# Optimization experiments

Hardware: AMD Instinct MI355X
Metric: run time of the kernel (lower is better)

The kernel has to match this reference:

```python
import jax, jax.numpy as jnp
import numpy as np
from jax import lax

EMBED = 768
D_INNER = 2 * EMBED          # expand = 2
D_STATE = 16
D_CONV = 4
DT_RANK = (EMBED + 15) // 16  # 48
FF = 3072
B, L = 2, 1024


def setup_inputs() -> dict:
    key = jax.random.key(0)
    ks = jax.random.split(key, 20)
    s = 0.02
    inp = {
        "x": jax.random.normal(ks[0], (B, L, EMBED), jnp.float32),
        # Mamba params
        "in_proj_w": jax.random.normal(ks[1], (2 * D_INNER, EMBED), jnp.float32) * s,
        "conv_w": jax.random.normal(ks[2], (D_INNER, 1, D_CONV), jnp.float32) * s,
        "conv_b": jnp.zeros((D_INNER,), jnp.float32),
        "x_proj_w": jax.random.normal(ks[3], (DT_RANK + 2 * D_STATE, D_INNER), jnp.float32) * s,
        "dt_proj_w": jax.random.normal(ks[4], (D_INNER, DT_RANK), jnp.float32) * s,
        "dt_proj_b": jax.random.normal(ks[5], (D_INNER,), jnp.float32) * s,
        "A_log": jnp.log(jnp.broadcast_to(jnp.arange(1, D_STATE + 1, dtype=jnp.float32), (D_INNER, D_STATE))),
        "D_param": jnp.ones((D_INNER,), jnp.float32),
        "out_proj_w": jax.random.normal(ks[6], (EMBED, D_INNER), jnp.float32) * s,
        # block params
        "ln1_w": jnp.ones((EMBED,), jnp.float32), "ln1_b": jnp.zeros((EMBED,), jnp.float32),
        "ln2_w": jnp.ones((EMBED,), jnp.float32), "ln2_b": jnp.zeros((EMBED,), jnp.float32),
        "ffn_w1": jax.random.normal(ks[7], (FF, EMBED), jnp.float32) * s,
        "ffn_b1": jnp.zeros((FF,), jnp.float32),
        "ffn_w2": jax.random.normal(ks[8], (EMBED, FF), jnp.float32) * s,
        "ffn_b2": jnp.zeros((EMBED,), jnp.float32),
    }
    return inp


def _layernorm(x, w, b, eps=1e-5):
    mu = jnp.mean(x, -1, keepdims=True)
    var = jnp.mean((x - mu) ** 2, -1, keepdims=True)
    return (x - mu) * lax.rsqrt(var + eps) * w + b


def _mamba(x, in_proj_w, conv_w, conv_b, x_proj_w, dt_proj_w, dt_proj_b,
           A_log, D_param, out_proj_w):
    # x: [B, L, E]
    xz = jnp.einsum('ble,de->bld', x, in_proj_w)          # [B,L,2*Di]
    xin, z = jnp.split(xz, 2, axis=-1)                    # [B,L,Di] each
    # causal depthwise conv over time
    xc = lax.conv_general_dilated(
        xin.transpose(0, 2, 1), conv_w, window_strides=(1,),
        padding=[(D_CONV - 1, 0)], feature_group_count=D_INNER,
        dimension_numbers=('NCH', 'OIH', 'NCH'))
    xc = (xc + conv_b[None, :, None]).transpose(0, 2, 1)  # [B,L,Di]
    xc = jax.nn.silu(xc)
    # input-dependent SSM params
    x_dbl = jnp.einsum('bld,rd->blr', xc, x_proj_w)       # [B,L,dt_rank+2n]
    dt, Bm, Cm = jnp.split(x_dbl, [DT_RANK, DT_RANK + D_STATE], axis=-1)
    delta = jax.nn.softplus(jnp.einsum('blr,dr->bld', dt, dt_proj_w) + dt_proj_b)
    A = -jnp.exp(A_log)                                   # [Di, n]
    deltaA = jnp.exp(jnp.einsum('bld,dn->bldn', delta, A))
    deltaBu = jnp.einsum('bld,bln,bld->bldn', delta, Bm, xc)

    def step(h, xs):
        dA, dBu, Ct = xs                                  # [B,Di,n],[B,Di,n],[B,n]
        h = dA * h + dBu
        y = jnp.einsum('bdn,bn->bd', h, Ct)
        return h, y

    h0 = jnp.zeros((x.shape[0], D_INNER, D_STATE), x.dtype)
    _, ys = lax.scan(step, h0, (deltaA.transpose(1, 0, 2, 3),
                                deltaBu.transpose(1, 0, 2, 3),
                                Cm.transpose(1, 0, 2)))
    y = ys.transpose(1, 0, 2)                             # [B,L,Di]
    y = y + xc * D_param
    y = y * jax.nn.silu(z)
    return jnp.einsum('bld,ed->ble', y, out_proj_w)


def reference(x, in_proj_w, conv_w, conv_b, x_proj_w, dt_proj_w, dt_proj_b,
              A_log, D_param, out_proj_w, ln1_w, ln1_b, ln2_w, ln2_b,
              ffn_w1, ffn_b1, ffn_w2, ffn_b2):
    # dropout is identity in eval mode
    h = _mamba(x, in_proj_w, conv_w, conv_b, x_proj_w, dt_proj_w, dt_proj_b,
               A_log, D_param, out_proj_w)
    x1 = _layernorm(h + x, ln1_w, ln1_b)
    f = jnp.einsum('ble,fe->blf', x1, ffn_w1) + ffn_b1
    f = jax.nn.gelu(f)
    f = jnp.einsum('blf,ef->ble', f, ffn_w2) + ffn_b2
    return _layernorm(f + x1, ln2_w, ln2_b)
```

## Files before the change

kernel.cpp:

```cpp
#include <hip/hip_runtime.h>
#include <math.h>

#define EMBED 768
#define DI 1536
#define DSTATE 16
#define DCONV 4
#define DTRANK 48
#define FF 3072
#define BATCH 2
#define SEQ 1024
#define NROWS (BATCH*SEQ)
#define TCH 32
#define NCH (SEQ/TCH)
#define DBLK 64

typedef __bf16 bf16x8 __attribute__((ext_vector_type(8)));
typedef float f32x4 __attribute__((ext_vector_type(4)));
typedef unsigned int u32x4 __attribute__((ext_vector_type(4)));

static __device__ __forceinline__ unsigned short f2b(float f) {
    union { float f; unsigned u; } v; v.f = f;
    unsigned r = v.u + 0x7FFFu + ((v.u >> 16) & 1u);
    return (unsigned short)(r >> 16);
}
static __device__ __forceinline__ float b2f(unsigned short s) {
    union { unsigned u; float f; } v; v.u = ((unsigned)s) << 16;
    return v.f;
}

#define GLOAD_LDS16(g, l) __builtin_amdgcn_global_load_lds( \
    (const __attribute__((address_space(1))) void*)(g), \
    (__attribute__((address_space(3))) void*)(l), 16, 0, 0)

template<int EPI, int KSPLIT>
__global__ __launch_bounds__(256)
void gemm_sk(const unsigned short* __restrict__ A,
             const unsigned short* __restrict__ W,
             float* __restrict__ C, unsigned short* __restrict__ Cb,
             float* __restrict__ part,
             int M, int N, int K,
             const float* __restrict__ bias)
{
    __shared__ alignas(16) unsigned short As[2][128 * 32];
    __shared__ alignas(16) unsigned short Ws[2][64 * 32];
    const int tid  = threadIdx.x;
    const int lane = tid & 63, wave = tid >> 6;
    const int bm = blockIdx.y * 128, bn = blockIdx.x * 64;
    const int kc = K / KSPLIT;
    const int kz = blockIdx.z * kc;
    const int ln = lane & 15, lg = lane >> 4;

    f32x4 acc[2][4];
    #pragma unroll
    for (int i = 0; i < 2; ++i)
        #pragma unroll
        for (int j = 0; j < 4; ++j)
            acc[i][j] = (f32x4){0.f, 0.f, 0.f, 0.f};

    const int ra = tid >> 2, ca = tid & 3;
    const int cs = (ca * 8) ^ ((ra & 3) << 3);
    const unsigned short* gA0 = A + (size_t)(bm + ra) * K + kz + cs;
    const unsigned short* gA1 = A + (size_t)(bm + ra + 64) * K + kz + cs;
    const unsigned short* gW  = W + (size_t)(bn + ra) * K + kz + cs;

#define STAGE(bf, kk) do { \
        GLOAD_LDS16(gA0 + (kk), &As[bf][wave * 512]); \
        GLOAD_LDS16(gA1 + (kk), &As[bf][2048 + wave * 512]); \
        GLOAD_LDS16(gW  + (kk), &Ws[bf][wave * 512]); \
    } while (0)

    STAGE(0, 0);
    __syncthreads();
    int buf = 0;
    for (int k0 = 0; k0 < kc; k0 += 32) {
        if (k0 + 32 < kc) STAGE(buf ^ 1, k0 + 32);
        bf16x8 af[2], wf[4];
        #pragma unroll
        for (int i = 0; i < 2; ++i) {
            int row = wave * 32 + i * 16 + ln;
            af[i] = *reinterpret_cast<const bf16x8*>(
                &As[buf][row * 32 + ((lg * 8) ^ ((row & 3) << 3))]);
        }
        #pragma unroll
        for (int j = 0; j < 4; ++j) {
            int row = j * 16 + ln;
            wf[j] = *reinterpret_cast<const bf16x8*>(
                &Ws[buf][row * 32 + ((lg * 8) ^ ((row & 3) << 3))]);
        }
        #pragma unroll
        for (int i = 0; i < 2; ++i)
            #pragma unroll
            for (int j = 0; j < 4; ++j)
                acc[i][j] = __builtin_amdgcn_mfma_f32_16x16x32_bf16(af[i], wf[j], acc[i][j], 0, 0, 0);
        __syncthreads();
        buf ^= 1;
    }
#undef STAGE

    if constexpr (KSPLIT > 1) {
        float* pb = part + (size_t)blockIdx.z * M * N;
        #pragma unroll
        for (int i = 0; i < 2; ++i)
            #pragma unroll
            for (int j = 0; j < 4; ++j) {
                int col = bn + j * 16 + ln;
                #pragma unroll
                for (int rr = 0; rr < 4; ++rr) {
                    int row = bm + wave * 32 + i * 16 + lg * 4 + rr;
                    pb[(size_t)row * N + col] = acc[i][j][rr];
                }
            }
    } else {
        #pragma unroll
        for (int i = 0; i < 2; ++i)
            #pragma unroll
            for (int j = 0; j < 4; ++j) {
                int col = bn + j * 16 + ln;
                #pragma unroll
                for (int rr = 0; rr < 4; ++rr) {
                    int row = bm + wave * 32 + i * 16 + lg * 4 + rr;
                    float v = acc[i][j][rr];
                    size_t o = (size_t)row * N + col;
                    if (EPI == 1) {
                        v += bias[col];
                        C[o] = (v > 20.f) ? v : log1pf(expf(v));
                    } else if (EPI == 3) {
                        v += bias[col];
                        float t = 0.7978845608028654f * (v + 0.044715f * v * v * v);
                        Cb[o] = f2b(0.5f * v * (1.f + tanhf(t)));
                    } else if (EPI == 6) {
                        Cb[o] = f2b(v);
                    } else {
                        C[o] = v;
                    }
                }
            }
    }
}

template<int KS, int BIAS>
__global__ __launch_bounds__(256)
void reduce_ln(const float* __restrict__ part, const float* __restrict__ resid,
               const float* __restrict__ bias,
               const float* __restrict__ w, const float* __restrict__ bb,
               float* __restrict__ out, unsigned short* __restrict__ outb)
{
    const int row = blockIdx.x;
    const size_t ro = (size_t)row * EMBED;
    const int i0 = threadIdx.x, i1 = i0 + 256, i2 = i0 + 512;
    float v0 = 0.f, v1 = 0.f, v2 = 0.f;
    #pragma unroll
    for (int z = 0; z < KS; ++z) {
        const float* p = part + (size_t)z * NROWS * EMBED + ro;
        v0 += p[i0]; v1 += p[i1]; v2 += p[i2];
    }
    if (BIAS) { v0 += bias[i0]; v1 += bias[i1]; v2 += bias[i2]; }
    v0 += resid[ro + i0]; v1 += resid[ro + i1]; v2 += resid[ro + i2];

    float s  = v0 + v1 + v2;
    float s2 = v0 * v0 + v1 * v1 + v2 * v2;
    #pragma unroll
    for (int m = 1; m < 64; m <<= 1) {
        s  += __shfl_xor(s,  m);
        s2 += __shfl_xor(s2, m);
    }
    __shared__ float sh1[4], sh2[4];
    int wv = threadIdx.x >> 6;
    if ((threadIdx.x & 63) == 0) { sh1[wv] = s; sh2[wv] = s2; }
    __syncthreads();
    float S1 = sh1[0] + sh1[1] + sh1[2] + sh1[3];
    float S2 = sh2[0] + sh2[1] + sh2[2] + sh2[3];
    float mu  = S1 * (1.f / EMBED);
    float var = S2 * (1.f / EMBED) - mu * mu;
    float rs  = rsqrtf(var + 1e-5f);
    float o0 = (v0 - mu) * rs * w[i0] + bb[i0];
    float o1 = (v1 - mu) * rs * w[i1] + bb[i1];
    float o2 = (v2 - mu) * rs * w[i2] + bb[i2];
    out[ro + i0] = o0; out[ro + i1] = o1; out[ro + i2] = o2;
    if (outb) {
        outb[ro + i0] = f2b(o0); outb[ro + i1] = f2b(o1); outb[ro + i2] = f2b(o2);
    }
}

__global__ __launch_bounds__(256)
void xproj_mfma(const unsigned short* __restrict__ A,
                const unsigned short* __restrict__ W,
                float* __restrict__ part)
{
    const int mt = blockIdx.x, s = blockIdx.y;
    const int lane = threadIdx.x & 63, wave = threadIdx.x >> 6;
    const int ln = lane & 15, lg = lane >> 4;
    const int row0 = mt * 128 + wave * 32;
    const int kb = s * 192;
    f32x4 acc[2][5];
    #pragma unroll
    for (int i = 0; i < 2; ++i)
        #pragma unroll
        for (int j = 0; j < 5; ++j)
            acc[i][j] = (f32x4){0.f, 0.f, 0.f, 0.f};

    for (int kk = 0; kk < 192; kk += 32) {
        const int k = kb + kk + lg * 8;
        bf16x8 af[2], wf[5];
        af[0] = *reinterpret_cast<const bf16x8*>(A + (size_t)(row0 + ln) * DI + k);
        af[1] = *reinterpret_cast<const bf16x8*>(A + (size_t)(row0 + 16 + ln) * DI + k);
        #pragma unroll
        for (int j = 0; j < 5; ++j)
            wf[j] = *reinterpret_cast<const bf16x8*>(W + (size_t)(j * 16 + ln) * DI + k);
        #pragma unroll
        for (int i = 0; i < 2; ++i)
            #pragma unroll
            for (int j = 0; j < 5; ++j)
                acc[i][j] = __builtin_amdgcn_mfma_f32_16x16x32_bf16(af[i], wf[j], acc[i][j], 0, 0, 0);
    }
    float* pb = part + (size_t)s * NROWS * 80;
    #pragma unroll
    for (int i = 0; i < 2; ++i)
        #pragma unroll
        for (int j = 0; j < 5; ++j)
            #pragma unroll
            for (int rr = 0; rr < 4; ++rr) {
                int row = row0 + i * 16 + lg * 4 + rr;
                int col = j * 16 + ln;
                pb[(size_t)row * 80 + col] = acc[i][j][rr];
            }
}

__global__ __launch_bounds__(256)
void xproj_reduce(const float* __restrict__ part, float* __restrict__ xdbl,
                  unsigned short* __restrict__ xdblb)
{
    int idx = blockIdx.x * 256 + threadIdx.x;
    float sum = 0.f;
    #pragma unroll
    for (int s = 0; s < 8; ++s) sum += part[(size_t)s * NROWS * 80 + idx];
    xdbl[idx] = sum;
    int col = idx % 80, row = idx / 80;
    if (col < 48)      xdblb[row * 64 + col] = f2b(sum);
    else if (col < 64) xdblb[row * 64 + col] = 0;
}

__global__ __launch_bounds__(256)
void cvt7_k(const float* __restrict__ x,  const float* __restrict__ w1,
            const float* __restrict__ w2, const float* __restrict__ w3,
            const float* __restrict__ w4, const float* __restrict__ w5,
            const float* __restrict__ w6,
            unsigned short* __restrict__ xb,  unsigned short* __restrict__ w1b,
            unsigned short* __restrict__ w2b, unsigned short* __restrict__ w3b,
            unsigned short* __restrict__ w4b, unsigned short* __restrict__ w5b,
            unsigned short* __restrict__ w6b)
{
    size_t i4 = ((size_t)blockIdx.x * 256 + threadIdx.x) * 4;
    if (i4 >= 9953280u) {
        int off = (int)(i4 - 9953280u);
        if (off >= 98304) return;
        int row = off >> 6, colb = off & 63;
        ushort4 u = {0, 0, 0, 0};
        if (colb < 48) {
            float4 v = *reinterpret_cast<const float4*>(w6 + row * 48 + colb);
            u.x = f2b(v.x); u.y = f2b(v.y); u.z = f2b(v.z); u.w = f2b(v.w);
        }
        *reinterpret_cast<ushort4*>(w6b + off) = u;
        return;
    }
    const float* src; unsigned short* dst; size_t off;
    if      (i4 < 1572864u) { src = x;  dst = xb;  off = i4; }
    else if (i4 < 3932160u) { src = w1; dst = w1b; off = i4 - 1572864u; }
    else if (i4 < 5111808u) { src = w2; dst = w2b; off = i4 - 3932160u; }
    else if (i4 < 7471104u) { src = w3; dst = w3b; off = i4 - 5111808u; }
    else if (i4 < 9830400u) { src = w4; dst = w4b; off = i4 - 7471104u; }
    else                    { src = w5; dst = w5b; off = i4 - 9830400u; }
    float4 v = *reinterpret_cast<const float4*>(src + off);
    ushort4 u;
    u.x = f2b(v.x); u.y = f2b(v.y); u.z = f2b(v.z); u.w = f2b(v.w);
    *reinterpret_cast<ushort4*>(dst + off) = u;
}

__global__ __launch_bounds__(256)
void conv_silu_k(const unsigned short* __restrict__ xz, const float* __restrict__ cw,
                 const float* __restrict__ cb, unsigned short* __restrict__ xcb)
{
    int q = blockIdx.x * 256 + threadIdx.x;
    int d4 = (q * 4) % DI;
    int bt = (q * 4) / DI;
    int t  = bt % SEQ;
    const unsigned short* base = xz + (size_t)bt * (2 * DI) + d4;
    float4 acc = *reinterpret_cast<const float4*>(cb + d4);
    float4 wv0 = *reinterpret_cast<const float4*>(cw + (d4 + 0) * 4);
    float4 wv1 = *reinterpret_cast<const float4*>(cw + (d4 + 1) * 4);
    float4 wv2 = *reinterpret_cast<const float4*>(cw + (d4 + 2) * 4);
    float4 wv3 = *reinterpret_cast<const float4*>(cw + (d4 + 3) * 4);
    {
        ushort4 r = *reinterpret_cast<const ushort4*>(base);
        acc.x += wv0.w * b2f(r.x); acc.y += wv1.w * b2f(r.y);
        acc.z += wv2.w * b2f(r.z); acc.w += wv3.w * b2f(r.w);
    }
    if (t >= 1) {
        ushort4 r = *reinterpret_cast<const ushort4*>(base - 2 * DI);
        acc.x += wv0.z * b2f(r.x); acc.y += wv1.z * b2f(r.y);
        acc.z += wv2.z * b2f(r.z); acc.w += wv3.z * b2f(r.w);
    }
    if (t >= 2) {
        ushort4 r = *reinterpret_cast<const ushort4*>(base - 4 * DI);
        acc.x += wv0.y * b2f(r.x); acc.y += wv1.y * b2f(r.y);
        acc.z += wv2.y * b2f(r.z); acc.w += wv3.y * b2f(r.w);
    }
    if (t >= 3) {
        ushort4 r = *reinterpret_cast<const ushort4*>(base - 6 * DI);
        acc.x += wv0.x * b2f(r.x); acc.y += wv1.x * b2f(r.y);
        acc.z += wv2.x * b2f(r.z); acc.w += wv3.x * b2f(r.w);
    }
    ushort4 u;
    u.x = f2b(acc.x / (1.f + __expf(-acc.x)));
    u.y = f2b(acc.y / (1.f + __expf(-acc.y)));
    u.z = f2b(acc.z / (1.f + __expf(-acc.z)));
    u.w = f2b(acc.w / (1.f + __expf(-acc.w)));
    *reinterpret_cast<ushort4*>(xcb + (size_t)bt * DI + d4) = u;
}

__global__ __launch_bounds__(256)
void scan2_a(const float* __restrict__ delta, const unsigned short* __restrict__ xcb,
             const float* __restrict__ xdbl,  const float* __restrict__ A_log,
             float* __restrict__ hfin, float* __restrict__ aprod)
{
    const int d0 = blockIdx.x * DBLK, ch = blockIdx.y, b = blockIdx.z;
    const int t0 = ch * TCH;
    __shared__ float del_s[TCH][DBLK + 4];
    __shared__ unsigned short xc_s[TCH][DBLK + 8];
    __shared__ float b_s[TCH][20];
    const int tid = threadIdx.x;
    {
        const int c4 = tid & 15, tr = tid >> 4;
        #pragma unroll
        for (int p = 0; p < 2; ++p) {
            int t = p * 16 + tr;
            size_t rowo = (size_t)(b * SEQ + t0 + t);
            *reinterpret_cast<float4*>(&del_s[t][c4 * 4]) =
                *reinterpret_cast<const float4*>(&delta[rowo * DI + d0 + c4 * 4]);
        }
        const int cz = tid & 7, tz = tid >> 3;
        size_t rz = (size_t)(b * SEQ + t0 + tz);
        *reinterpret_cast<u32x4*>(&xc_s[tz][cz * 8]) =
            *reinterpret_cast<const u32x4*>(&xcb[rz * DI + d0 + cz * 8]);
        const int cbq = tid & 3, tb = tid >> 2;
        if (tb < TCH) {
            size_t rowo = (size_t)(b * SEQ + t0 + tb);
            *reinterpret_cast<float4*>(&b_s[tb][cbq * 4]) =
                *reinterpret_cast<const float4*>(&xdbl[rowo * 80 + DTRANK + cbq * 4]);
        }
    }
    __syncthreads();
    const int lane = tid & 63, wave = tid >> 6;
    const int wd = wave * 16 + (lane >> 2);
    const int d = d0 + wd;
    const int nq = (lane & 3) * 4;
    float4 Av = *reinterpret_cast<const float4*>(&A_log[d * DSTATE + nq]);
    const float A0 = -__expf(Av.x), A1 = -__expf(Av.y), A2 = -__expf(Av.z), A3 = -__expf(Av.w);
    float h0_ = 0.f, h1_ = 0.f, h2_ = 0.f, h3_ = 0.f;
    float p0 = 1.f, p1 = 1.f, p2 = 1.f, p3 = 1.f;
    #pragma unroll 4
    for (int t = 0; t < TCH; ++t) {
        float dl = del_s[t][wd];
        float u  = dl * b2f(xc_s[t][wd]);
        float4 bq = *reinterpret_cast<const float4*>(&b_s[t][nq]);
        float e0 = __expf(dl * A0), e1 = __expf(dl * A1);
        float e2 = __expf(dl * A2), e3 = __expf(dl * A3);
        h0_ = e0 * h0_ + u * bq.x; p0 *= e0;
        h1_ = e1 * h1_ + u * bq.y; p1 *= e1;
        h2_ = e2 * h2_ + u * bq.z; p2 *= e2;
        h3_ = e3 * h3_ + u * bq.w; p3 *= e3;
    }
    size_t o = ((size_t)((b * NCH + ch) * DI) + d) * DSTATE + nq;
    *reinterpret_cast<float4*>(&hfin[o])  = (float4){h0_, h1_, h2_, h3_};
    *reinterpret_cast<float4*>(&aprod[o]) = (float4){p0, p1, p2, p3};
}

__global__ __launch_bounds__(256)
void scan2_c(const float* __restrict__ delta, const unsigned short* __restrict__ xcb,
             const float* __restrict__ xdbl,  const float* __restrict__ A_log,
             const float* __restrict__ Dp,    const unsigned short* __restrict__ xz,
             const float* __restrict__ hfin,  const float* __restrict__ aprod,
             unsigned short* __restrict__ yb)
{
    const int d0 = blockIdx.x * DBLK, ch = blockIdx.y, b = blockIdx.z;
    const int t0 = ch * TCH;
    __shared__ float del_s[TCH][DBLK + 4];
    __shared__ unsigned short xc_s[TCH][DBLK + 8];
    __shared__ float b_s[TCH][20];
    __shared__ float c_s[TCH][20];
    __shared__ unsigned short z_s[TCH][DBLK + 8];
    const int tid = threadIdx.x;
    {
        const int c4 = tid & 15, tr = tid >> 4;
        #pragma unroll
        for (int p = 0; p < 2; ++p) {
            int t = p * 16 + tr;
            size_t rowo = (size_t)(b * SEQ + t0 + t);
            *reinterpret_cast<float4*>(&del_s[t][c4 * 4]) =
                *reinterpret_cast<const float4*>(&delta[rowo * DI + d0 + c4 * 4]);
        }
        const int cz = tid & 7, tz = tid >> 3;
        size_t rz = (size_t)(b * SEQ + t0 + tz);
        *reinterpret_cast<u32x4*>(&xc_s[tz][cz * 8]) =
            *reinterpret_cast<const u32x4*>(&xcb[rz * DI + d0 + cz * 8]);
        *reinterpret_cast<u32x4*>(&z_s[tz][cz * 8]) =
            *reinterpret_cast<const u32x4*>(&xz[rz * (2 * DI) + DI + d0 + cz * 8]);
        const int cbq = tid & 3, tb = tid >> 2;
        if (tb < TCH) {
            size_t rowo = (size_t)(b * SEQ + t0 + tb);
            *reinterpret_cast<float4*>(&b_s[tb][cbq * 4]) =
                *reinterpret_cast<const float4*>(&xdbl[rowo * 80 + DTRANK + cbq * 4]);
        } else {
            size_t rowo = (size_t)(b * SEQ + t0 + tb - TCH);
            *reinterpret_cast<float4*>(&c_s[tb - TCH][cbq * 4]) =
                *reinterpret_cast<const float4*>(&xdbl[rowo * 80 + DTRANK + DSTATE + cbq * 4]);
        }
    }
    const int lane = tid & 63, wave = tid >> 6;
    const int wd = wave * 16 + (lane >> 2);
    const int d = d0 + wd;
    const int nq = (lane & 3) * 4;

    float4 h = {0.f, 0.f, 0.f, 0.f};
    for (int cc = 0; cc < ch; ++cc) {
        size_t o = ((size_t)((b * NCH + cc) * DI) + d) * DSTATE + nq;
        float4 a = *reinterpret_cast<const float4*>(&aprod[o]);
        float4 f = *reinterpret_cast<const float4*>(&hfin[o]);
        h.x = a.x * h.x + f.x; h.y = a.y * h.y + f.y;
        h.z = a.z * h.z + f.z; h.w = a.w * h.w + f.w;
    }

    float4 Av = *reinterpret_cast<const float4*>(&A_log[d * DSTATE + nq]);
    const float A0 = -__expf(Av.x), A1 = -__expf(Av.y), A2 = -__expf(Av.z), A3 = -__expf(Av.w);
    const float Dd = Dp[d];
    __syncthreads();
    unsigned short* yrow = yb + (size_t)(b * SEQ + t0) * DI + d;
    #pragma unroll 4
    for (int t = 0; t < TCH; ++t) {
        float dl = del_s[t][wd];
        float xv = b2f(xc_s[t][wd]);
        float u  = dl * xv;
        float4 bq = *reinterpret_cast<const float4*>(&b_s[t][nq]);
        float4 cq = *reinterpret_cast<const float4*>(&c_s[t][nq]);
        float e0 = __expf(dl * A0), e1 = __expf(dl * A1);
        float e2 = __expf(dl * A2), e3 = __expf(dl * A3);
        h.x = e0 * h.x + u * bq.x;
        h.y = e1 * h.y + u * bq.y;
        h.z = e2 * h.z + u * bq.z;
        h.w = e3 * h.w + u * bq.w;
        float py = h.x * cq.x + h.y * cq.y + h.z * cq.z + h.w * cq.w;
        py += __shfl_xor(py, 1);
        py += __shfl_xor(py, 2);
        if ((lane & 3) == 0) {
            float yv = py + xv * Dd;
            float zv = b2f(z_s[t][wd]);
            yv *= zv / (1.f + __expf(-zv));
            yrow[(size_t)t * DI] = f2b(yv);
        }
    }
}

extern "C" void kernel_launch(void* const* d_in, const int* in_sizes, int n_in,
                              void* d_out, int out_size, void* d_ws, size_t ws_size,
                              hipStream_t stream)
{
    const float* x         = (const float*)d_in[0];
    const float* in_proj_w = (const float*)d_in[1];
    const float* conv_w    = (const float*)d_in[2];
    const float* conv_b    = (const float*)d_in[3];
    const float* x_proj_w  = (const float*)d_in[4];
    const float* dt_proj_w = (const float*)d_in[5];
    const float* dt_proj_b = (const float*)d_in[6];
    const float* A_log     = (const float*)d_in[7];
    const float* D_param   = (const float*)d_in[8];
    const float* out_proj_w= (const float*)d_in[9];
    const float* ln1_w     = (const float*)d_in[10];
    const float* ln1_b     = (const float*)d_in[11];
    const float* ln2_w     = (const float*)d_in[12];
    const float* ln2_b     = (const float*)d_in[13];
    const float* ffn_w1    = (const float*)d_in[14];
    const float* ffn_b1    = (const float*)d_in[15];
    const float* ffn_w2    = (const float*)d_in[16];
    const float* ffn_b2    = (const float*)d_in[17];
    float* out = (float*)d_out;

    char* Wp = (char*)d_ws;
    #define MB(n) ((size_t)(n) * 1048576)
    unsigned short* xzb   = (unsigned short*)(Wp + 0);
    unsigned short* xcb   = (unsigned short*)(Wp + MB(16));
    float*          xdbl  = (float*)         (Wp + MB(24));
    unsigned short* xdblb = (unsigned short*)(Wp + MB(26));
    float*          delta = (float*)         (Wp + MB(28));
    unsigned short* ybb   = (unsigned short*)(Wp + MB(42));
    float*          hfin  = (float*)         (Wp + MB(50));
    float*          aprod = (float*)         (Wp + MB(58));
    unsigned short* xb    = (unsigned short*)(Wp + MB(66));
    unsigned short* wib   = (unsigned short*)(Wp + MB(70));
    unsigned short* wob   = (unsigned short*)(Wp + MB(75));
    unsigned short* wf1b  = (unsigned short*)(Wp + MB(78));
    unsigned short* wf2b  = (unsigned short*)(Wp + MB(83));
    unsigned short* xpwb  = (unsigned short*)(Wp + MB(88));
    unsigned short* wdtb  = (unsigned short*)(Wp + MB(89));
    float*          part  = (float*)         (Wp + MB(90));
    float*          part_op = (float*)       (Wp + MB(96));
    float*          part_f2 = (float*)       (Wp + MB(122));
    float*          x1    = (float*)         (Wp + MB(148));
    unsigned short* x1b   = (unsigned short*)(Wp + MB(155));
    unsigned short* fbf   = (unsigned short*)(Wp + MB(159));
    #undef MB

    dim3 blk(256);

    cvt7_k<<<9816, blk, 0, stream>>>(x, in_proj_w, out_proj_w, ffn_w1, ffn_w2, x_proj_w,
                                     dt_proj_w, xb, wib, wob, wf1b, wf2b, xpwb, wdtb);

    gemm_sk<6, 1><<<dim3(48, 16, 1), blk, 0, stream>>>(xb, wib, nullptr, xzb, nullptr,
                                                       NROWS, 2 * DI, EMBED, nullptr);

    conv_silu_k<<<(BATCH * SEQ * DI) / 1024, blk, 0, stream>>>(xzb, conv_w, conv_b, xcb);

    xproj_mfma<<<dim3(16, 8), blk, 0, stream>>>(xcb, xpwb, part);
    xproj_reduce<<<640, blk, 0, stream>>>(part, xdbl, xdblb);

    gemm_sk<1, 1><<<dim3(24, 16, 1), blk, 0, stream>>>(xdblb, wdtb, delta, nullptr, nullptr,
                                                       NROWS, DI, 64, dt_proj_b);

    scan2_a<<<dim3(DI / DBLK, NCH, BATCH), blk, 0, stream>>>(delta, xcb, xdbl, A_log, hfin, aprod);
    scan2_c<<<dim3(DI / DBLK, NCH, BATCH), blk, 0, stream>>>(delta, xcb, xdbl, A_log, D_param,
                                                             xzb, hfin, aprod, ybb);

    gemm_sk<0, 4><<<dim3(12, 16, 4), blk, 0, stream>>>(ybb, wob, nullptr, nullptr, part_op,
                                                       NROWS, EMBED, DI, nullptr);
    reduce_ln<4, 0><<<NROWS, blk, 0, stream>>>(part_op, x, nullptr, ln1_w, ln1_b, x1, x1b);

    gemm_sk<3, 1><<<dim3(48, 16, 1), blk, 0, stream>>>(x1b, wf1b, nullptr, fbf, nullptr,
                                                       NROWS, FF, EMBED, ffn_b1);

    gemm_sk<0, 4><<<dim3(12, 16, 4), blk, 0, stream>>>(fbf, wf2b, nullptr, nullptr, part_f2,
                                                       NROWS, EMBED, FF, nullptr);
    reduce_ln<4, 1><<<NROWS, blk, 0, stream>>>(part_f2, x1, ffn_b2, ln2_w, ln2_b, out, nullptr);
}
```

Measured before the change: 201.5 us.

## Fuse dt_proj GEMM and softplus into both scan kernels via MFMA

Removes the separate dt_proj GEMM launch and the fp32 delta buffer. Each scan block now computes its own 32x64 delta tile from the bf16 x_dbl and dt weights with MFMA plus softplus, writing it to shared memory. This cuts a kernel launch and the 12MB write plus two reads of delta, at the cost of computing delta twice (once in each scan pass) and adding extra syncs.

```diff
diff --git a/kernel.cpp b/kernel.cpp
--- a/kernel.cpp
+++ b/kernel.cpp
@@ -121,10 +121,7 @@
                     int row = bm + wave * 32 + i * 16 + lg * 4 + rr;
                     float v = acc[i][j][rr];
                     size_t o = (size_t)row * N + col;
-                    if (EPI == 1) {
-                        v += bias[col];
-                        C[o] = (v > 20.f) ? v : log1pf(expf(v));
-                    } else if (EPI == 3) {
+                    if (EPI == 3) {
                         v += bias[col];
                         float t = 0.7978845608028654f * (v + 0.044715f * v * v * v);
                         Cb[o] = f2b(0.5f * v * (1.f + tanhf(t)));
@@ -318,30 +315,55 @@
     *reinterpret_cast<ushort4*>(xcb + (size_t)bt * DI + d4) = u;
 }
 
-__global__ __launch_bounds__(256)
-void scan2_a(const float* __restrict__ delta, const unsigned short* __restrict__ xcb,
-             const float* __restrict__ xdbl,  const float* __restrict__ A_log,
+static __device__ __forceinline__ void dt_mfma(
+    const unsigned short (*xd_s)[72], float (*del_s)[DBLK + 4],
+    const unsigned short* __restrict__ wdtb, const float* __restrict__ dtb,
+    int d0, int wave, int ln, int lg)
+{
+    f32x4 dacc[2];
+    dacc[0] = (f32x4){0.f, 0.f, 0.f, 0.f};
+    dacc[1] = (f32x4){0.f, 0.f, 0.f, 0.f};
+    const unsigned short* wrow = wdtb + (size_t)(d0 + wave * 16 + ln) * 64;
+    #pragma unroll
+    for (int kk = 0; kk < 2; ++kk) {
+        bf16x8 wf = *reinterpret_cast<const bf16x8*>(wrow + kk * 32 + lg * 8);
+        #pragma unroll
+        for (int i = 0; i < 2; ++i) {
+            bf16x8 a = *reinterpret_cast<const bf16x8*>(&xd_s[i * 16 + ln][kk * 32 + lg * 8]);
+            dacc[i] = __builtin_amdgcn_mfma_f32_16x16x32_bf16(a, wf, dacc[i], 0, 0, 0);
+        }
+    }
+    float bias_d = dtb[d0 + wave * 16 + ln];
+    #pragma unroll
+    for (int i = 0; i < 2; ++i)
+        #pragma unroll
+        for (int rr = 0; rr < 4; ++rr) {
+            float v = dacc[i][rr] + bias_d;
+            del_s[i * 16 + lg * 4 + rr][wave * 16 + ln] =
+                (v > 20.f) ? v : log1pf(__expf(v));
+        }
+}
+
+__global__ __launch_bounds__(256)
+void scan2_a(const unsigned short* __restrict__ xdblb, const unsigned short* __restrict__ wdtb,
+             const float* __restrict__ dtb,  const unsigned short* __restrict__ xcb,
+             const float* __restrict__ xdbl, const float* __restrict__ A_log,
              float* __restrict__ hfin, float* __restrict__ aprod)
 {
     const int d0 = blockIdx.x * DBLK, ch = blockIdx.y, b = blockIdx.z;
     const int t0 = ch * TCH;
     __shared__ float del_s[TCH][DBLK + 4];
+    __shared__ unsigned short xd_s[TCH][72];
     __shared__ unsigned short xc_s[TCH][DBLK + 8];
     __shared__ float b_s[TCH][20];
     const int tid = threadIdx.x;
     {
-        const int c4 = tid & 15, tr = tid >> 4;
-        #pragma unroll
-        for (int p = 0; p < 2; ++p) {
-            int t = p * 16 + tr;
-            size_t rowo = (size_t)(b * SEQ + t0 + t);
-            *reinterpret_cast<float4*>(&del_s[t][c4 * 4]) =
-                *reinterpret_cast<const float4*>(&delta[rowo * DI + d0 + c4 * 4]);
-        }
         const int cz = tid & 7, tz = tid >> 3;
         size_t rz = (size_t)(b * SEQ + t0 + tz);
         *reinterpret_cast<u32x4*>(&xc_s[tz][cz * 8]) =
             *reinterpret_cast<const u32x4*>(&xcb[rz * DI + d0 + cz * 8]);
+        *reinterpret_cast<u32x4*>(&xd_s[tz][cz * 8]) =
+            *reinterpret_cast<const u32x4*>(&xdblb[rz * 64 + cz * 8]);
         const int cbq = tid & 3, tb = tid >> 2;
         if (tb < TCH) {
             size_t rowo = (size_t)(b * SEQ + t0 + tb);
@@ -351,6 +373,10 @@
     }
     __syncthreads();
     const int lane = tid & 63, wave = tid >> 6;
+    const int ln = lane & 15, lg = lane >> 4;
+    dt_mfma(xd_s, del_s, wdtb, dtb, d0, wave, ln, lg);
+    __syncthreads();
+
     const int wd = wave * 16 + (lane >> 2);
     const int d = d0 + wd;
     const int nq = (lane & 3) * 4;
@@ -376,35 +402,31 @@
 }
 
 __global__ __launch_bounds__(256)
-void scan2_c(const float* __restrict__ delta, const unsigned short* __restrict__ xcb,
-             const float* __restrict__ xdbl,  const float* __restrict__ A_log,
-             const float* __restrict__ Dp,    const unsigned short* __restrict__ xz,
-             const float* __restrict__ hfin,  const float* __restrict__ aprod,
+void scan2_c(const unsigned short* __restrict__ xdblb, const unsigned short* __restrict__ wdtb,
+             const float* __restrict__ dtb,  const unsigned short* __restrict__ xcb,
+             const float* __restrict__ xdbl, const float* __restrict__ A_log,
+             const float* __restrict__ Dp,   const unsigned short* __restrict__ xz,
+             const float* __restrict__ hfin, const float* __restrict__ aprod,
              unsigned short* __restrict__ yb)
 {
     const int d0 = blockIdx.x * DBLK, ch = blockIdx.y, b = blockIdx.z;
     const int t0 = ch * TCH;
     __shared__ float del_s[TCH][DBLK + 4];
+    __shared__ unsigned short xd_s[TCH][72];
     __shared__ unsigned short xc_s[TCH][DBLK + 8];
     __shared__ float b_s[TCH][20];
     __shared__ float c_s[TCH][20];
     __shared__ unsigned short z_s[TCH][DBLK + 8];
     const int tid = threadIdx.x;
     {
-        const int c4 = tid & 15, tr = tid >> 4;
-        #pragma unroll
-        for (int p = 0; p < 2; ++p) {
-            int t = p * 16 + tr;
-            size_t rowo = (size_t)(b * SEQ + t0 + t);
-            *reinterpret_cast<float4*>(&del_s[t][c4 * 4]) =
-                *reinterpret_cast<const float4*>(&delta[rowo * DI + d0 + c4 * 4]);
-        }
         const int cz = tid & 7, tz = tid >> 3;
         size_t rz = (size_t)(b * SEQ + t0 + tz);
         *reinterpret_cast<u32x4*>(&xc_s[tz][cz * 8]) =
             *reinterpret_cast<const u32x4*>(&xcb[rz * DI + d0 + cz * 8]);
         *reinterpret_cast<u32x4*>(&z_s[tz][cz * 8]) =
             *reinterpret_cast<const u32x4*>(&xz[rz * (2 * DI) + DI + d0 + cz * 8]);
+        *reinterpret_cast<u32x4*>(&xd_s[tz][cz * 8]) =
+            *reinterpret_cast<const u32x4*>(&xdblb[rz * 64 + cz * 8]);
         const int cbq = tid & 3, tb = tid >> 2;
         if (tb < TCH) {
             size_t rowo = (size_t)(b * SEQ + t0 + tb);
@@ -417,6 +439,7 @@
         }
     }
     const int lane = tid & 63, wave = tid >> 6;
+    const int ln = lane & 15, lg = lane >> 4;
     const int wd = wave * 16 + (lane >> 2);
     const int d = d0 + wd;
     const int nq = (lane & 3) * 4;
@@ -430,10 +453,13 @@
         h.z = a.z * h.z + f.z; h.w = a.w * h.w + f.w;
     }
 
+    __syncthreads();
+    dt_mfma(xd_s, del_s, wdtb, dtb, d0, wave, ln, lg);
+    __syncthreads();
+
     float4 Av = *reinterpret_cast<const float4*>(&A_log[d * DSTATE + nq]);
     const float A0 = -__expf(Av.x), A1 = -__expf(Av.y), A2 = -__expf(Av.z), A3 = -__expf(Av.w);
     const float Dd = Dp[d];
-    __syncthreads();
     unsigned short* yrow = yb + (size_t)(b * SEQ + t0) * DI + d;
     #pragma unroll 4
     for (int t = 0; t < TCH; ++t) {
@@ -490,23 +516,22 @@
     unsigned short* xcb   = (unsigned short*)(Wp + MB(16));
     float*          xdbl  = (float*)         (Wp + MB(24));
     unsigned short* xdblb = (unsigned short*)(Wp + MB(26));
-    float*          delta = (float*)         (Wp + MB(28));
-    unsigned short* ybb   = (unsigned short*)(Wp + MB(42));
-    float*          hfin  = (float*)         (Wp + MB(50));
-    float*          aprod = (float*)         (Wp + MB(58));
-    unsigned short* xb    = (unsigned short*)(Wp + MB(66));
-    unsigned short* wib   = (unsigned short*)(Wp + MB(70));
-    unsigned short* wob   = (unsigned short*)(Wp + MB(75));
-    unsigned short* wf1b  = (unsigned short*)(Wp + MB(78));
-    unsigned short* wf2b  = (unsigned short*)(Wp + MB(83));
-    unsigned short* xpwb  = (unsigned short*)(Wp + MB(88));
-    unsigned short* wdtb  = (unsigned short*)(Wp + MB(89));
-    float*          part  = (float*)         (Wp + MB(90));
-    float*          part_op = (float*)       (Wp + MB(96));
-    float*          part_f2 = (float*)       (Wp + MB(122));
-    float*          x1    = (float*)         (Wp + MB(148));
-    unsigned short* x1b   = (unsigned short*)(Wp + MB(155));
-    unsigned short* fbf   = (unsigned short*)(Wp + MB(159));
+    unsigned short* ybb   = (unsigned short*)(Wp + MB(28));
+    float*          hfin  = (float*)         (Wp + MB(36));
+    float*          aprod = (float*)         (Wp + MB(44));
+    unsigned short* xb    = (unsigned short*)(Wp + MB(52));
+    unsigned short* wib   = (unsigned short*)(Wp + MB(56));
+    unsigned short* wob   = (unsigned short*)(Wp + MB(61));
+    unsigned short* wf1b  = (unsigned short*)(Wp + MB(64));
+    unsigned short* wf2b  = (unsigned short*)(Wp + MB(69));
+    unsigned short* xpwb  = (unsigned short*)(Wp + MB(74));
+    unsigned short* wdtb  = (unsigned short*)(Wp + MB(75));
+    float*          part  = (float*)         (Wp + MB(76));
+    float*          part_op = (float*)       (Wp + MB(82));
+    float*          part_f2 = (float*)       (Wp + MB(108));
+    float*          x1    = (float*)         (Wp + MB(134));
+    unsigned short* x1b   = (unsigned short*)(Wp + MB(141));
+    unsigned short* fbf   = (unsigned short*)(Wp + MB(145));
     #undef MB
 
     dim3 blk(256);
@@ -522,12 +547,10 @@
     xproj_mfma<<<dim3(16, 8), blk, 0, stream>>>(xcb, xpwb, part);
     xproj_reduce<<<640, blk, 0, stream>>>(part, xdbl, xdblb);
 
-    gemm_sk<1, 1><<<dim3(24, 16, 1), blk, 0, stream>>>(xdblb, wdtb, delta, nullptr, nullptr,
-                                                       NROWS, DI, 64, dt_proj_b);
-
-    scan2_a<<<dim3(DI / DBLK, NCH, BATCH), blk, 0, stream>>>(delta, xcb, xdbl, A_log, hfin, aprod);
-    scan2_c<<<dim3(DI / DBLK, NCH, BATCH), blk, 0, stream>>>(delta, xcb, xdbl, A_log, D_param,
-                                                             xzb, hfin, aprod, ybb);
+    scan2_a<<<dim3(DI / DBLK, NCH, BATCH), blk, 0, stream>>>(
+        xdblb, wdtb, dt_proj_b, xcb, xdbl, A_log, hfin, aprod);
+    scan2_c<<<dim3(DI / DBLK, NCH, BATCH), blk, 0, stream>>>(
+        xdblb, wdtb, dt_proj_b, xcb, xdbl, A_log, D_param, xzb, hfin, aprod, ybb);
 
     gemm_sk<0, 4><<<dim3(12, 16, 4), blk, 0, stream>>>(ybb, wob, nullptr, nullptr, part_op,
                                                        NROWS, EMBED, DI, nullptr);
```

New measurement: 203.6 us. About the same (+1.0%).
